# Performance work log

Hardware: AMD Instinct MI355X
Metric: run time of the kernel (lower is better)

Reference implementation:

```python
import jax, jax.numpy as jnp
import numpy as np

B, H, W, C = 32, 32, 32, 256


def setup_inputs() -> dict:
    key = jax.random.key(0)
    k1, k2 = jax.random.split(key)
    feats1 = jax.random.normal(k1, (B, H, W, C), dtype=jnp.float32)
    feats2 = jax.random.normal(k2, (B, H, W, C), dtype=jnp.float32)
    return {"feats1": feats1, "feats2": feats2}


def reference(feats1, feats2):
    # Training path of LocalFeatureLoss (trainflag=True)
    b, h, w, c = feats1.shape
    l = h * w
    q = feats1.reshape(b, l, c)  # queries: (B, l, C)
    p = feats2.reshape(b, l, c)  # preds:   (B, l, C)
    # M[b, a, j] = <p[b,a], q[b,j]>  == fm2 @ fm1.T per batch
    M = jnp.einsum('bac,bjc->baj', p, q)  # (B, l_pred, l_query)
    max1 = jnp.argmax(M, axis=1)  # (B, l_q): best pred index for each query token
    max2 = jnp.argmax(M, axis=2)  # (B, l_p): best query index for each pred token
    # mutual nearest-neighbor check: m[b, j] = max2[b, max1[b, j]]
    m = jnp.take_along_axis(max2, max1, axis=1)  # (B, l_q)
    valid = jnp.arange(l)[None, :] == m          # (B, l_q) bool
    # gather matched pred descriptors and compute per-pair similarity
    matched_p = jnp.take_along_axis(p, max1[..., None], axis=1)  # (B, l_q, C)
    sims = jnp.sum(q * matched_p, axis=-1)                        # (B, l_q)
    cnt = jnp.sum(valid, axis=1).astype(sims.dtype)               # (B,)
    # mean over mutual NN pairs (torch mean over idx1)
    similarity = jnp.sum(jnp.where(valid, sims, 0.0), axis=1) / jnp.maximum(cnt, 1.0)
    return similarity
```

## Files before the change

kernel.cpp:

```cpp
#include <hip/hip_runtime.h>
#include <hip/hip_bf16.h>

#define BATCH 32
#define L 1024
#define CD 256
#define NRT 8
#define NCT 16
#define PAN_A 32768
#define TILE_B 16384

typedef __bf16 bf16x8 __attribute__((ext_vector_type(8)));
typedef float  f32x4  __attribute__((ext_vector_type(4)));
typedef unsigned long long u64;

__device__ __forceinline__ unsigned int enc_f32(float f) {
    unsigned int u = __float_as_uint(f);
    return ((int)u < 0) ? ~u : (u | 0x80000000u);
}
__device__ __forceinline__ float dec_f32(unsigned int u) {
    u = (u & 0x80000000u) ? (u & 0x7FFFFFFFu) : ~u;
    return __uint_as_float(u);
}
__device__ __forceinline__ u64 pmax(u64 a, u64 b) { return a > b ? a : b; }

__device__ __forceinline__ void gl_lds16(const __bf16* g, __bf16* l) {
    __builtin_amdgcn_global_load_lds(
        (const __attribute__((address_space(1))) unsigned int*)g,
        (__attribute__((address_space(3))) unsigned int*)l, 16, 0, 0);
}

__global__ __launch_bounds__(256) void convert_kernel(
    const float* __restrict__ qg,
    const float* __restrict__ pg,
    __bf16* __restrict__ qsw,
    __bf16* __restrict__ psw)
{
    const unsigned int t = blockIdx.x * 256 + threadIdx.x;
    const unsigned int v = t & ((1u << 20) - 1);
    const bool isQ = (t >> 20) != 0;

    const float* src;
    __bf16* dst;
    if (isQ) {
        const int s    = v & 7;
        const int row  = (v >> 3) & 63;
        const int step = (v >> 9) & 3;
        const int ct   = (v >> 11) & 15;
        const int b    = v >> 15;
        src = qg + ((size_t)(b * L + ct * 64 + row)) * CD
                 + step * 64 + ((s ^ (row & 7)) * 8);
        dst = qsw + (size_t)v * 8;
    } else {
        const int s    = v & 7;
        const int row  = (v >> 3) & 127;
        const int step = (v >> 10) & 3;
        const int pan  = (v >> 12) & 7;
        const int b    = v >> 15;
        src = pg + ((size_t)(b * L + pan * 128 + row)) * CD
                 + step * 64 + ((s ^ (row & 7)) * 8);
        dst = psw + (size_t)v * 8;
    }
    const float4 f0 = *(const float4*)src;
    const float4 f1 = *(const float4*)(src + 4);
    bf16x8 o;
    o[0] = (__bf16)f0.x; o[1] = (__bf16)f0.y; o[2] = (__bf16)f0.z; o[3] = (__bf16)f0.w;
    o[4] = (__bf16)f1.x; o[5] = (__bf16)f1.y; o[6] = (__bf16)f1.z; o[7] = (__bf16)f1.w;
    *(bf16x8*)&dst[0] = o;
}

__global__ __launch_bounds__(512, 2) void mm_argmax_kernel(
    const __bf16* __restrict__ qsw,
    const __bf16* __restrict__ psw,
    u64* __restrict__ colpart,
    int* __restrict__ max2)
{
    __shared__ __bf16 sA[4 * 8192];
    __shared__ __bf16 sB[2][4 * 4096];
    __shared__ u64 sRow[2][128];

    const int tid = threadIdx.x;
    const int bid = blockIdx.x;
    const int b  = bid & 31;
    const int rt = bid >> 5;

    const int lane = tid & 63;
    const int w    = tid >> 6;
    const int wm   = w >> 1;
    const int wn   = w & 1;
    const int quad = lane >> 4;
    const int l16  = lane & 15;

    const __bf16* pa  = psw + (size_t)(b * NRT + rt) * PAN_A;
    const __bf16* pbb = qsw + (size_t)b * NCT * TILE_B;

    #pragma unroll
    for (int c = 0; c < 8; ++c)
        gl_lds16(pa + c * 4096 + tid * 8, &sA[c * 4096 + tid * 8]);
    #pragma unroll
    for (int c = 0; c < 4; ++c)
        gl_lds16(pbb + c * 4096 + tid * 8, &sB[0][c * 4096 + tid * 8]);
    #pragma unroll
    for (int c = 0; c < 4; ++c)
        gl_lds16(pbb + TILE_B + c * 4096 + tid * 8, &sB[1][c * 4096 + tid * 8]);

    f32x4 acc[2][2];
    float rowv[2][4];
    int   rowj[2][4];
    #pragma unroll
    for (int tm = 0; tm < 2; ++tm)
        #pragma unroll
        for (int r = 0; r < 4; ++r) { rowv[tm][r] = -1e30f; rowj[tm][r] = 0; }

    asm volatile("s_waitcnt vmcnt(4)" ::: "memory");
    __builtin_amdgcn_s_barrier();
    __builtin_amdgcn_sched_barrier(0);

    const size_t colbase = ((size_t)(b * NRT + rt) * 4 + wm) * L;
    const int a0q = rt * 128 + wm * 32 + quad * 4;

    for (int t = 0; t < NCT; ++t) {
        const __bf16* sBb = sB[t & 1];
        #pragma unroll
        for (int tm = 0; tm < 2; ++tm)
            #pragma unroll
            for (int tn = 0; tn < 2; ++tn) acc[tm][tn] = (f32x4){0.f, 0.f, 0.f, 0.f};

        __builtin_amdgcn_s_setprio(1);
        #pragma unroll
        for (int step = 0; step < 4; ++step) {
            #pragma unroll
            for (int kk = 0; kk < 2; ++kk) {
                const int sw = ((kk * 4 + quad) ^ (l16 & 7)) << 3;
                bf16x8 a0 = *(const bf16x8*)&sA [step * 8192 + (wm * 32      + l16) * 64 + sw];
                bf16x8 a1 = *(const bf16x8*)&sA [step * 8192 + (wm * 32 + 16 + l16) * 64 + sw];
                bf16x8 b0 = *(const bf16x8*)&sBb[step * 4096 + (wn * 32      + l16) * 64 + sw];
                bf16x8 b1 = *(const bf16x8*)&sBb[step * 4096 + (wn * 32 + 16 + l16) * 64 + sw];
                acc[0][0] = __builtin_amdgcn_mfma_f32_16x16x32_bf16(a0, b0, acc[0][0], 0, 0, 0);
                acc[0][1] = __builtin_amdgcn_mfma_f32_16x16x32_bf16(a0, b1, acc[0][1], 0, 0, 0);
                acc[1][0] = __builtin_amdgcn_mfma_f32_16x16x32_bf16(a1, b0, acc[1][0], 0, 0, 0);
                acc[1][1] = __builtin_amdgcn_mfma_f32_16x16x32_bf16(a1, b1, acc[1][1], 0, 0, 0);
            }
        }
        __builtin_amdgcn_s_setprio(0);

        const int jb = t * 64 + wn * 32 + l16;
        #pragma unroll
        for (int tm = 0; tm < 2; ++tm)
            #pragma unroll
            for (int r = 0; r < 4; ++r) {
                const float v0 = acc[tm][0][r], v1 = acc[tm][1][r];
                if (v0 > rowv[tm][r]) { rowv[tm][r] = v0; rowj[tm][r] = jb; }
                if (v1 > rowv[tm][r]) { rowv[tm][r] = v1; rowj[tm][r] = jb + 16; }
            }

        #pragma unroll
        for (int tn = 0; tn < 2; ++tn) {
            float cv = acc[0][tn][0];
            int   ca = a0q;
            #pragma unroll
            for (int r = 1; r < 4; ++r)
                if (acc[0][tn][r] > cv) { cv = acc[0][tn][r]; ca = a0q + r; }
            #pragma unroll
            for (int r = 0; r < 4; ++r)
                if (acc[1][tn][r] > cv) { cv = acc[1][tn][r]; ca = a0q + 16 + r; }
            u64 pk = ((u64)enc_f32(cv) << 32) | (unsigned int)(~(unsigned int)ca);
            pk = pmax(pk, __shfl_xor(pk, 16));
            pk = pmax(pk, __shfl_xor(pk, 32));
            if (quad == 0)
                colpart[colbase + t * 64 + wn * 32 + tn * 16 + l16] = pk;
        }

        __builtin_amdgcn_s_barrier();
        __builtin_amdgcn_sched_barrier(0);
        if (t + 2 < NCT) {
            #pragma unroll
            for (int c = 0; c < 4; ++c)
                gl_lds16(pbb + (size_t)(t + 2) * TILE_B + c * 4096 + tid * 8,
                         &sB[t & 1][c * 4096 + tid * 8]);
        }
        if (t < NCT - 1) {
            if (t + 2 < NCT) { asm volatile("s_waitcnt vmcnt(6)" ::: "memory"); }
            else             { asm volatile("s_waitcnt vmcnt(2)" ::: "memory"); }
            __builtin_amdgcn_s_barrier();
            __builtin_amdgcn_sched_barrier(0);
        }
    }

    #pragma unroll
    for (int tm = 0; tm < 2; ++tm)
        #pragma unroll
        for (int r = 0; r < 4; ++r) {
            u64 pk = ((u64)enc_f32(rowv[tm][r]) << 32)
                   | (unsigned int)(~(unsigned int)rowj[tm][r]);
            pk = pmax(pk, __shfl_xor(pk, 1));
            pk = pmax(pk, __shfl_xor(pk, 2));
            pk = pmax(pk, __shfl_xor(pk, 4));
            pk = pmax(pk, __shfl_xor(pk, 8));
            if (l16 == 0) sRow[wn][wm * 32 + tm * 16 + quad * 4 + r] = pk;
        }
    __syncthreads();
    if (tid < 128) {
        const u64 m = pmax(sRow[0][tid], sRow[1][tid]);
        max2[(size_t)b * L + rt * 128 + tid] = (int)(~(unsigned int)m) & (L - 1);
    }
}

__global__ __launch_bounds__(1024) void finalize_kernel(
    const u64* __restrict__ colpart,
    const int* __restrict__ max2,
    float* __restrict__ out)
{
    __shared__ int sMax2[L];
    __shared__ float sSum[16];
    __shared__ int sCnt[16];
    const int b = blockIdx.x;
    const int j = threadIdx.x;

    sMax2[j] = max2[(size_t)b * L + j];

    u64 cb = 0ull;
    #pragma unroll
    for (int k = 0; k < 32; ++k)
        cb = pmax(cb, colpart[((size_t)b * 32 + k) * L + j]);
    __syncthreads();

    const int a = (int)(~(unsigned int)cb) & (L - 1);
    const float val = dec_f32((unsigned int)(cb >> 32));
    const bool mut = (sMax2[a] == j);
    float sum = mut ? val : 0.f;
    int   cnt = mut ? 1 : 0;

    #pragma unroll
    for (int o = 32; o >= 1; o >>= 1) {
        sum += __shfl_down(sum, o);
        cnt += __shfl_down(cnt, o);
    }
    if ((j & 63) == 0) { sSum[j >> 6] = sum; sCnt[j >> 6] = cnt; }
    __syncthreads();
    if (j == 0) {
        float S = 0.f;
        int   C = 0;
        #pragma unroll
        for (int i = 0; i < 16; ++i) { S += sSum[i]; C += sCnt[i]; }
        out[b] = S / fmaxf((float)C, 1.0f);
    }
}

extern "C" void kernel_launch(void* const* d_in, const int* in_sizes, int n_in,
                              void* d_out, int out_size, void* d_ws, size_t ws_size,
                              hipStream_t stream) {
    const float* q = (const float*)d_in[0];
    const float* p = (const float*)d_in[1];
    float* out = (float*)d_out;

    u64* colpart = (u64*)d_ws;
    int* max2 = (int*)(colpart + (size_t)BATCH * 32 * L);
    __bf16* psw = (__bf16*)((char*)d_ws + 8 * 1024 * 1024 + 512 * 1024);
    __bf16* qsw = psw + (size_t)BATCH * NRT * PAN_A;

    convert_kernel<<<8192, 256, 0, stream>>>(q, p, qsw, psw);
    mm_argmax_kernel<<<BATCH * NRT, 512, 0, stream>>>(qsw, psw, colpart, max2);
    finalize_kernel<<<BATCH, 1024, 0, stream>>>(colpart, max2, out);
}
```

Measured before the change: 141.0 us.

## Hold A fragments in registers, widen B tiles, reduce column partials in LDS

The pred (A) panel is pre-laid out by the convert kernel in MFMA fragment order, so each wave loads its 64x256 slice straight into 32 registers instead of staging it in LDS and re-reading it every tile. Waves are rearranged 2x4 with 64 rows each and B tiles grow to 128 columns, giving 8 fully unrolled double-buffered iterations. Column argmax partials are merged across waves in LDS before one write per block, which cuts colpart traffic and the finalize reduction from 32 to 8 entries per column. The cost is much higher register pressure (afr plus acc) under the 512x2 launch bounds, and LDS use goes to 64KB for sB plus 18KB for the reduction buffers, which may spill or lower occupancy.

Measured after the change: 185.2 us. 1.31x slower.

```diff
diff --git a/kernel.cpp b/kernel.cpp
--- a/kernel.cpp
+++ b/kernel.cpp
@@ -5,9 +5,8 @@
 #define L 1024
 #define CD 256
 #define NRT 8
-#define NCT 16
-#define PAN_A 32768
-#define TILE_B 16384
+#define NBT 8
+#define TILE_B 32768
 
 typedef __bf16 bf16x8 __attribute__((ext_vector_type(8)));
 typedef float  f32x4  __attribute__((ext_vector_type(4)));
@@ -33,50 +32,52 @@
     const float* __restrict__ qg,
     const float* __restrict__ pg,
     __bf16* __restrict__ qsw,
-    __bf16* __restrict__ psw)
+    __bf16* __restrict__ areg)
 {
     const unsigned int t = blockIdx.x * 256 + threadIdx.x;
-    const unsigned int v = t & ((1u << 20) - 1);
-    const bool isQ = (t >> 20) != 0;
-
+    const unsigned int v = t & 0xFFFFFu;
     const float* src;
     __bf16* dst;
-    if (isQ) {
+    if (t >> 20) {
         const int s    = v & 7;
-        const int row  = (v >> 3) & 63;
-        const int step = (v >> 9) & 3;
-        const int ct   = (v >> 11) & 15;
+        const int crow = (v >> 3) & 127;
+        const int step = (v >> 10) & 3;
+        const int ct   = (v >> 12) & 7;
         const int b    = v >> 15;
-        src = qg + ((size_t)(b * L + ct * 64 + row)) * CD
-                 + step * 64 + ((s ^ (row & 7)) * 8);
+        src = qg + ((size_t)(b << 10) + (ct << 7) + crow) * CD
+                 + (step << 6) + ((s ^ (crow & 7)) << 3);
         dst = qsw + (size_t)v * 8;
     } else {
-        const int s    = v & 7;
-        const int row  = (v >> 3) & 127;
-        const int step = (v >> 10) & 3;
-        const int pan  = (v >> 12) & 7;
+        const int ln   = v & 63;
+        const int f    = (v >> 6) & 31;
+        const int wmv  = (v >> 11) & 1;
+        const int rtv  = (v >> 12) & 7;
         const int b    = v >> 15;
-        src = pg + ((size_t)(b * L + pan * 128 + row)) * CD
-                 + step * 64 + ((s ^ (row & 7)) * 8);
-        dst = psw + (size_t)v * 8;
+        const int tm   = f >> 3;
+        const int step = (f >> 1) & 3;
+        const int kk   = f & 1;
+        const int row  = (rtv << 7) + (wmv << 6) + (tm << 4) + (ln & 15);
+        const int k    = (step << 6) + (((kk << 2) + (ln >> 4)) << 3);
+        src = pg + ((size_t)(b << 10) + row) * CD + k;
+        dst = areg + (size_t)v * 8;
     }
     const float4 f0 = *(const float4*)src;
     const float4 f1 = *(const float4*)(src + 4);
     bf16x8 o;
     o[0] = (__bf16)f0.x; o[1] = (__bf16)f0.y; o[2] = (__bf16)f0.z; o[3] = (__bf16)f0.w;
     o[4] = (__bf16)f1.x; o[5] = (__bf16)f1.y; o[6] = (__bf16)f1.z; o[7] = (__bf16)f1.w;
-    *(bf16x8*)&dst[0] = o;
+    *(bf16x8*)dst = o;
 }
 
 __global__ __launch_bounds__(512, 2) void mm_argmax_kernel(
     const __bf16* __restrict__ qsw,
-    const __bf16* __restrict__ psw,
+    const __bf16* __restrict__ areg,
     u64* __restrict__ colpart,
     int* __restrict__ max2)
 {
-    __shared__ __bf16 sA[4 * 8192];
-    __shared__ __bf16 sB[2][4 * 4096];
-    __shared__ u64 sRow[2][128];
+    __shared__ __bf16 sB[2][TILE_B];
+    __shared__ u64 sColW[2][L];
+    __shared__ u64 sRowW[4][128];
 
     const int tid = threadIdx.x;
     const int bid = blockIdx.x;
@@ -85,109 +86,122 @@
 
     const int lane = tid & 63;
     const int w    = tid >> 6;
-    const int wm   = w >> 1;
-    const int wn   = w & 1;
+    const int wm   = w >> 2;
+    const int wn   = w & 3;
     const int quad = lane >> 4;
     const int l16  = lane & 15;
 
-    const __bf16* pa  = psw + (size_t)(b * NRT + rt) * PAN_A;
-    const __bf16* pbb = qsw + (size_t)b * NCT * TILE_B;
+    const __bf16* qb = qsw + (size_t)b * NBT * TILE_B;
+    const __bf16* ab = areg + (size_t)((b * NRT + rt) * 2 + wm) * 32 * 512;
+
+    bf16x8 afr[32];
+    #pragma unroll
+    for (int f = 0; f < 32; ++f)
+        afr[f] = *(const bf16x8*)&ab[f * 512 + lane * 8];
+    __builtin_amdgcn_sched_barrier(0);
 
     #pragma unroll
     for (int c = 0; c < 8; ++c)
-        gl_lds16(pa + c * 4096 + tid * 8, &sA[c * 4096 + tid * 8]);
-    #pragma unroll
-    for (int c = 0; c < 4; ++c)
-        gl_lds16(pbb + c * 4096 + tid * 8, &sB[0][c * 4096 + tid * 8]);
-    #pragma unroll
-    for (int c = 0; c < 4; ++c)
-        gl_lds16(pbb + TILE_B + c * 4096 + tid * 8, &sB[1][c * 4096 + tid * 8]);
-
-    f32x4 acc[2][2];
-    float rowv[2][4];
-    int   rowj[2][4];
-    #pragma unroll
-    for (int tm = 0; tm < 2; ++tm)
+        gl_lds16(qb + c * 4096 + tid * 8, &sB[0][c * 4096 + tid * 8]);
+    __builtin_amdgcn_sched_barrier(0);
+    #pragma unroll
+    for (int c = 0; c < 8; ++c)
+        gl_lds16(qb + TILE_B + c * 4096 + tid * 8, &sB[1][c * 4096 + tid * 8]);
+    __builtin_amdgcn_sched_barrier(0);
+
+    f32x4 acc[4][2];
+    float rowv[4][4];
+    int   rowj[4][4];
+    #pragma unroll
+    for (int tm = 0; tm < 4; ++tm)
         #pragma unroll
         for (int r = 0; r < 4; ++r) { rowv[tm][r] = -1e30f; rowj[tm][r] = 0; }
 
-    asm volatile("s_waitcnt vmcnt(4)" ::: "memory");
-    __builtin_amdgcn_s_barrier();
-    __builtin_amdgcn_sched_barrier(0);
-
-    const size_t colbase = ((size_t)(b * NRT + rt) * 4 + wm) * L;
-    const int a0q = rt * 128 + wm * 32 + quad * 4;
-
-    for (int t = 0; t < NCT; ++t) {
-        const __bf16* sBb = sB[t & 1];
-        #pragma unroll
-        for (int tm = 0; tm < 2; ++tm)
-            #pragma unroll
-            for (int tn = 0; tn < 2; ++tn) acc[tm][tn] = (f32x4){0.f, 0.f, 0.f, 0.f};
-
-        __builtin_amdgcn_s_setprio(1);
-        #pragma unroll
-        for (int step = 0; step < 4; ++step) {
-            #pragma unroll
-            for (int kk = 0; kk < 2; ++kk) {
-                const int sw = ((kk * 4 + quad) ^ (l16 & 7)) << 3;
-                bf16x8 a0 = *(const bf16x8*)&sA [step * 8192 + (wm * 32      + l16) * 64 + sw];
-                bf16x8 a1 = *(const bf16x8*)&sA [step * 8192 + (wm * 32 + 16 + l16) * 64 + sw];
-                bf16x8 b0 = *(const bf16x8*)&sBb[step * 4096 + (wn * 32      + l16) * 64 + sw];
-                bf16x8 b1 = *(const bf16x8*)&sBb[step * 4096 + (wn * 32 + 16 + l16) * 64 + sw];
-                acc[0][0] = __builtin_amdgcn_mfma_f32_16x16x32_bf16(a0, b0, acc[0][0], 0, 0, 0);
-                acc[0][1] = __builtin_amdgcn_mfma_f32_16x16x32_bf16(a0, b1, acc[0][1], 0, 0, 0);
-                acc[1][0] = __builtin_amdgcn_mfma_f32_16x16x32_bf16(a1, b0, acc[1][0], 0, 0, 0);
-                acc[1][1] = __builtin_amdgcn_mfma_f32_16x16x32_bf16(a1, b1, acc[1][1], 0, 0, 0);
-            }
+    const int a0q = rt * 128 + wm * 64 + quad * 4;
+
+    #define COMPUTE(T)                                                         \
+    {                                                                          \
+        const __bf16* sBb = sB[(T) & 1];                                       \
+        _Pragma("unroll")                                                      \
+        for (int tm = 0; tm < 4; ++tm)                                         \
+            _Pragma("unroll")                                                  \
+            for (int tn = 0; tn < 2; ++tn) acc[tm][tn] = (f32x4){0.f,0.f,0.f,0.f}; \
+        __builtin_amdgcn_s_setprio(1);                                         \
+        _Pragma("unroll")                                                      \
+        for (int step = 0; step < 4; ++step) {                                 \
+            _Pragma("unroll")                                                  \
+            for (int kk = 0; kk < 2; ++kk) {                                   \
+                const int sw = ((kk * 4 + quad) ^ (l16 & 7)) << 3;             \
+                bf16x8 b0 = *(const bf16x8*)&sBb[step * 8192 + (wn * 32      + l16) * 64 + sw]; \
+                bf16x8 b1 = *(const bf16x8*)&sBb[step * 8192 + (wn * 32 + 16 + l16) * 64 + sw]; \
+                _Pragma("unroll")                                              \
+                for (int tm = 0; tm < 4; ++tm) {                               \
+                    acc[tm][0] = __builtin_amdgcn_mfma_f32_16x16x32_bf16(      \
+                        afr[tm * 8 + step * 2 + kk], b0, acc[tm][0], 0, 0, 0); \
+                    acc[tm][1] = __builtin_amdgcn_mfma_f32_16x16x32_bf16(      \
+                        afr[tm * 8 + step * 2 + kk], b1, acc[tm][1], 0, 0, 0); \
+                }                                                              \
+            }                                                                  \
+        }                                                                      \
+        __builtin_amdgcn_s_setprio(0);                                         \
+         \
+        const int jb = (T) * 128 + wn * 32 + l16;                              \
+        _Pragma("unroll")                                                      \
+        for (int tm = 0; tm < 4; ++tm)                                         \
+            _Pragma("unroll")                                                  \
+            for (int r = 0; r < 4; ++r) {                                      \
+                const float v0 = acc[tm][0][r], v1 = acc[tm][1][r];            \
+                if (v0 > rowv[tm][r]) { rowv[tm][r] = v0; rowj[tm][r] = jb; }  \
+                if (v1 > rowv[tm][r]) { rowv[tm][r] = v1; rowj[tm][r] = jb + 16; } \
+            }                                                                  \
+          \
+        _Pragma("unroll")                                                      \
+        for (int tn = 0; tn < 2; ++tn) {                                       \
+            float cv = acc[0][tn][0];                                          \
+            int   ca = a0q;                                                    \
+            _Pragma("unroll")                                                  \
+            for (int tm = 0; tm < 4; ++tm)                                     \
+                _Pragma("unroll")                                              \
+                for (int r = 0; r < 4; ++r) {                                  \
+                    if (tm == 0 && r == 0) continue;                           \
+                    if (acc[tm][tn][r] > cv) { cv = acc[tm][tn][r]; ca = a0q + tm * 16 + r; } \
+                }                                                              \
+            u64 pk = ((u64)enc_f32(cv) << 32) | (unsigned int)(~(unsigned int)ca); \
+            pk = pmax(pk, __shfl_xor(pk, 16));                                 \
+            pk = pmax(pk, __shfl_xor(pk, 32));                                 \
+            if (quad == 0) sColW[wm][(T) * 128 + wn * 32 + tn * 16 + l16] = pk; \
+        }                                                                      \
+    }
+
+    #define TILE_ITER(T, VM)                                                   \
+        asm volatile("s_waitcnt vmcnt(" #VM ")" ::: "memory");                 \
+        __builtin_amdgcn_s_barrier();                                          \
+        __builtin_amdgcn_sched_barrier(0);                                     \
+        COMPUTE(T)                                                             \
+        __builtin_amdgcn_s_barrier();                                          \
+        __builtin_amdgcn_sched_barrier(0);                                     \
+        if ((T) + 2 < NBT) {                                                   \
+            _Pragma("unroll")                                                  \
+            for (int c = 0; c < 8; ++c)                                        \
+                gl_lds16(qb + (size_t)((T) + 2) * TILE_B + c * 4096 + tid * 8, \
+                         &sB[(T) & 1][c * 4096 + tid * 8]);                    \
+            __builtin_amdgcn_sched_barrier(0);                                 \
         }
-        __builtin_amdgcn_s_setprio(0);
-
-        const int jb = t * 64 + wn * 32 + l16;
-        #pragma unroll
-        for (int tm = 0; tm < 2; ++tm)
-            #pragma unroll
-            for (int r = 0; r < 4; ++r) {
-                const float v0 = acc[tm][0][r], v1 = acc[tm][1][r];
-                if (v0 > rowv[tm][r]) { rowv[tm][r] = v0; rowj[tm][r] = jb; }
-                if (v1 > rowv[tm][r]) { rowv[tm][r] = v1; rowj[tm][r] = jb + 16; }
-            }
-
-        #pragma unroll
-        for (int tn = 0; tn < 2; ++tn) {
-            float cv = acc[0][tn][0];
-            int   ca = a0q;
-            #pragma unroll
-            for (int r = 1; r < 4; ++r)
-                if (acc[0][tn][r] > cv) { cv = acc[0][tn][r]; ca = a0q + r; }
-            #pragma unroll
-            for (int r = 0; r < 4; ++r)
-                if (acc[1][tn][r] > cv) { cv = acc[1][tn][r]; ca = a0q + 16 + r; }
-            u64 pk = ((u64)enc_f32(cv) << 32) | (unsigned int)(~(unsigned int)ca);
-            pk = pmax(pk, __shfl_xor(pk, 16));
-            pk = pmax(pk, __shfl_xor(pk, 32));
-            if (quad == 0)
-                colpart[colbase + t * 64 + wn * 32 + tn * 16 + l16] = pk;
-        }
-
-        __builtin_amdgcn_s_barrier();
-        __builtin_amdgcn_sched_barrier(0);
-        if (t + 2 < NCT) {
-            #pragma unroll
-            for (int c = 0; c < 4; ++c)
-                gl_lds16(pbb + (size_t)(t + 2) * TILE_B + c * 4096 + tid * 8,
-                         &sB[t & 1][c * 4096 + tid * 8]);
-        }
-        if (t < NCT - 1) {
-            if (t + 2 < NCT) { asm volatile("s_waitcnt vmcnt(6)" ::: "memory"); }
-            else             { asm volatile("s_waitcnt vmcnt(2)" ::: "memory"); }
-            __builtin_amdgcn_s_barrier();
-            __builtin_amdgcn_sched_barrier(0);
-        }
-    }
-
-    #pragma unroll
-    for (int tm = 0; tm < 2; ++tm)
+
+    TILE_ITER(0, 8)
+    TILE_ITER(1, 8)
+    TILE_ITER(2, 8)
+    TILE_ITER(3, 8)
+    TILE_ITER(4, 8)
+    TILE_ITER(5, 8)
+    TILE_ITER(6, 8)
+    TILE_ITER(7, 0)
+
+    #undef TILE_ITER
+    #undef COMPUTE
+
+    #pragma unroll
+    for (int tm = 0; tm < 4; ++tm)
         #pragma unroll
         for (int r = 0; r < 4; ++r) {
             u64 pk = ((u64)enc_f32(rowv[tm][r]) << 32)
@@ -196,12 +210,18 @@
             pk = pmax(pk, __shfl_xor(pk, 2));
             pk = pmax(pk, __shfl_xor(pk, 4));
             pk = pmax(pk, __shfl_xor(pk, 8));
-            if (l16 == 0) sRow[wn][wm * 32 + tm * 16 + quad * 4 + r] = pk;
+            if (l16 == 0) sRowW[wn][wm * 64 + tm * 16 + quad * 4 + r] = pk;
         }
     __syncthreads();
     if (tid < 128) {
-        const u64 m = pmax(sRow[0][tid], sRow[1][tid]);
+        const u64 m = pmax(pmax(sRowW[0][tid], sRowW[1][tid]),
+                           pmax(sRowW[2][tid], sRowW[3][tid]));
         max2[(size_t)b * L + rt * 128 + tid] = (int)(~(unsigned int)m) & (L - 1);
+    }
+    #pragma unroll
+    for (int c0 = 0; c0 < 2; ++c0) {
+        const int c = c0 * 512 + tid;
+        colpart[(size_t)(b * NRT + rt) * L + c] = pmax(sColW[0][c], sColW[1][c]);
     }
 }
 
@@ -220,8 +240,8 @@
 
     u64 cb = 0ull;
     #pragma unroll
-    for (int k = 0; k < 32; ++k)
-        cb = pmax(cb, colpart[((size_t)b * 32 + k) * L + j]);
+    for (int k = 0; k < NRT; ++k)
+        cb = pmax(cb, colpart[(size_t)(b * NRT + k) * L + j]);
     __syncthreads();
 
     const int a = (int)(~(unsigned int)cb) & (L - 1);
@@ -254,11 +274,11 @@
     float* out = (float*)d_out;
 
     u64* colpart = (u64*)d_ws;
-    int* max2 = (int*)(colpart + (size_t)BATCH * 32 * L);
-    __bf16* psw = (__bf16*)((char*)d_ws + 8 * 1024 * 1024 + 512 * 1024);
-    __bf16* qsw = psw + (size_t)BATCH * NRT * PAN_A;
-
-    convert_kernel<<<8192, 256, 0, stream>>>(q, p, qsw, psw);
-    mm_argmax_kernel<<<BATCH * NRT, 512, 0, stream>>>(qsw, psw, colpart, max2);
+    int* max2 = (int*)(colpart + (size_t)BATCH * NRT * L);
+    __bf16* areg = (__bf16*)((char*)d_ws + (2u << 20) + (128u << 10));
+    __bf16* qsw = areg + (size_t)8388608;
+
+    convert_kernel<<<8192, 256, 0, stream>>>(q, p, qsw, areg);
+    mm_argmax_kernel<<<BATCH * NRT, 512, 0, stream>>>(qsw, areg, colpart, max2);
     finalize_kernel<<<BATCH, 1024, 0, stream>>>(colpart, max2, out);
 }
```

## Fuse fp32-to-bf16 conversion into matmul-argmax kernel with register-prefetched Q tiles

Applied to the files above, without the earlier changes.

Removes the separate conversion kernel and its bf16 round trip through global memory. The matmul kernel now loads fp32 feats directly, converts to bf16 in registers, and writes swizzled tiles to LDS. Q tiles are prefetched into registers one K-step ahead. Tiling changes to 64-row pred panels with 256-thread blocks (512 blocks) and 128-column query tiles split over K steps. Each block re-reads and re-converts the Q fp32 data (16x per batch), and the loads go through VGPRs instead of direct-to-LDS, which adds register pressure and barrier stalls.

Result: no change. 142.8 us (+1.3%).

```diff
diff --git a/kernel.cpp b/kernel.cpp
--- a/kernel.cpp
+++ b/kernel.cpp
@@ -4,10 +4,8 @@
 #define BATCH 32
 #define L 1024
 #define CD 256
-#define NRT 8
-#define NCT 16
-#define PAN_A 32768
-#define TILE_B 16384
+#define NRT 16
+#define NQT 32
 
 typedef __bf16 bf16x8 __attribute__((ext_vector_type(8)));
 typedef float  f32x4  __attribute__((ext_vector_type(4)));
@@ -22,61 +20,24 @@
     return __uint_as_float(u);
 }
 __device__ __forceinline__ u64 pmax(u64 a, u64 b) { return a > b ? a : b; }
-
-__device__ __forceinline__ void gl_lds16(const __bf16* g, __bf16* l) {
-    __builtin_amdgcn_global_load_lds(
-        (const __attribute__((address_space(1))) unsigned int*)g,
-        (__attribute__((address_space(3))) unsigned int*)l, 16, 0, 0);
-}
-
-__global__ __launch_bounds__(256) void convert_kernel(
+__device__ __forceinline__ bf16x8 cvt8(float4 a, float4 b) {
+    bf16x8 o;
+    o[0] = (__bf16)a.x; o[1] = (__bf16)a.y; o[2] = (__bf16)a.z; o[3] = (__bf16)a.w;
+    o[4] = (__bf16)b.x; o[5] = (__bf16)b.y; o[6] = (__bf16)b.z; o[7] = (__bf16)b.w;
+    return o;
+}
+
+__global__ void __launch_bounds__(256)
+__attribute__((amdgpu_waves_per_eu(2)))
+mm_argmax_kernel(
     const float* __restrict__ qg,
     const float* __restrict__ pg,
-    __bf16* __restrict__ qsw,
-    __bf16* __restrict__ psw)
-{
-    const unsigned int t = blockIdx.x * 256 + threadIdx.x;
-    const unsigned int v = t & ((1u << 20) - 1);
-    const bool isQ = (t >> 20) != 0;
-
-    const float* src;
-    __bf16* dst;
-    if (isQ) {
-        const int s    = v & 7;
-        const int row  = (v >> 3) & 63;
-        const int step = (v >> 9) & 3;
-        const int ct   = (v >> 11) & 15;
-        const int b    = v >> 15;
-        src = qg + ((size_t)(b * L + ct * 64 + row)) * CD
-                 + step * 64 + ((s ^ (row & 7)) * 8);
-        dst = qsw + (size_t)v * 8;
-    } else {
-        const int s    = v & 7;
-        const int row  = (v >> 3) & 127;
-        const int step = (v >> 10) & 3;
-        const int pan  = (v >> 12) & 7;
-        const int b    = v >> 15;
-        src = pg + ((size_t)(b * L + pan * 128 + row)) * CD
-                 + step * 64 + ((s ^ (row & 7)) * 8);
-        dst = psw + (size_t)v * 8;
-    }
-    const float4 f0 = *(const float4*)src;
-    const float4 f1 = *(const float4*)(src + 4);
-    bf16x8 o;
-    o[0] = (__bf16)f0.x; o[1] = (__bf16)f0.y; o[2] = (__bf16)f0.z; o[3] = (__bf16)f0.w;
-    o[4] = (__bf16)f1.x; o[5] = (__bf16)f1.y; o[6] = (__bf16)f1.z; o[7] = (__bf16)f1.w;
-    *(bf16x8*)&dst[0] = o;
-}
-
-__global__ __launch_bounds__(512, 2) void mm_argmax_kernel(
-    const __bf16* __restrict__ qsw,
-    const __bf16* __restrict__ psw,
     u64* __restrict__ colpart,
     int* __restrict__ max2)
 {
-    __shared__ __bf16 sA[4 * 8192];
-    __shared__ __bf16 sB[2][4 * 4096];
-    __shared__ u64 sRow[2][128];
+    __shared__ __bf16 sA[4 * 4096];
+    __shared__ __bf16 sB[2][8192];
+    __shared__ u64 sRow[2][64];
 
     const int tid = threadIdx.x;
     const int bid = blockIdx.x;
@@ -90,108 +51,163 @@
     const int quad = lane >> 4;
     const int l16  = lane & 15;
 
-    const __bf16* pa  = psw + (size_t)(b * NRT + rt) * PAN_A;
-    const __bf16* pbb = qsw + (size_t)b * NCT * TILE_B;
-
-    #pragma unroll
-    for (int c = 0; c < 8; ++c)
-        gl_lds16(pa + c * 4096 + tid * 8, &sA[c * 4096 + tid * 8]);
-    #pragma unroll
-    for (int c = 0; c < 4; ++c)
-        gl_lds16(pbb + c * 4096 + tid * 8, &sB[0][c * 4096 + tid * 8]);
-    #pragma unroll
-    for (int c = 0; c < 4; ++c)
-        gl_lds16(pbb + TILE_B + c * 4096 + tid * 8, &sB[1][c * 4096 + tid * 8]);
-
-    f32x4 acc[2][2];
-    float rowv[2][4];
-    int   rowj[2][4];
+    const float* pA = pg + ((size_t)b * L + rt * 64) * CD;
+    const float* pQ = qg + (size_t)b * L * CD;
+
+    #pragma unroll
+    for (int pass = 0; pass < 2; ++pass) {
+        float4 t[8];
+        #pragma unroll
+        for (int s = 0; s < 4; ++s) {
+            const int sid = (pass * 4 + s) * 256 + tid;
+            const int row = sid >> 5;
+            const int ks  = (sid >> 3) & 3;
+            const int sl  = sid & 7;
+            const float* src = pA + row * CD + ks * 64 + ((sl ^ (row & 7)) << 3);
+            t[2 * s]     = ((const float4*)src)[0];
+            t[2 * s + 1] = ((const float4*)src)[1];
+        }
+        #pragma unroll
+        for (int s = 0; s < 4; ++s) {
+            const int sid = (pass * 4 + s) * 256 + tid;
+            const int row = sid >> 5;
+            const int ks  = (sid >> 3) & 3;
+            const int sl  = sid & 7;
+            *(bf16x8*)&sA[ks * 4096 + row * 64 + sl * 8] = cvt8(t[2 * s], t[2 * s + 1]);
+        }
+    }
+    {
+        float4 t[8];
+        #pragma unroll
+        for (int s = 0; s < 4; ++s) {
+            const int sid  = s * 256 + tid;
+            const int crow = sid >> 3;
+            const int sl   = sid & 7;
+            const float* src = pQ + (size_t)crow * CD + ((sl ^ (crow & 7)) << 3);
+            t[2 * s]     = ((const float4*)src)[0];
+            t[2 * s + 1] = ((const float4*)src)[1];
+        }
+        #pragma unroll
+        for (int s = 0; s < 4; ++s) {
+            const int sid  = s * 256 + tid;
+            const int crow = sid >> 3;
+            const int sl   = sid & 7;
+            *(bf16x8*)&sB[0][crow * 64 + sl * 8] = cvt8(t[2 * s], t[2 * s + 1]);
+        }
+    }
+
+    f32x4 acc[2][4];
+    u64 rowbest[2][4];
     #pragma unroll
     for (int tm = 0; tm < 2; ++tm)
         #pragma unroll
-        for (int r = 0; r < 4; ++r) { rowv[tm][r] = -1e30f; rowj[tm][r] = 0; }
-
-    asm volatile("s_waitcnt vmcnt(4)" ::: "memory");
-    __builtin_amdgcn_s_barrier();
-    __builtin_amdgcn_sched_barrier(0);
-
-    const size_t colbase = ((size_t)(b * NRT + rt) * 4 + wm) * L;
-    const int a0q = rt * 128 + wm * 32 + quad * 4;
-
-    for (int t = 0; t < NCT; ++t) {
-        const __bf16* sBb = sB[t & 1];
-        #pragma unroll
-        for (int tm = 0; tm < 2; ++tm)
-            #pragma unroll
-            for (int tn = 0; tn < 2; ++tn) acc[tm][tn] = (f32x4){0.f, 0.f, 0.f, 0.f};
-
-        __builtin_amdgcn_s_setprio(1);
-        #pragma unroll
-        for (int step = 0; step < 4; ++step) {
-            #pragma unroll
-            for (int kk = 0; kk < 2; ++kk) {
-                const int sw = ((kk * 4 + quad) ^ (l16 & 7)) << 3;
-                bf16x8 a0 = *(const bf16x8*)&sA [step * 8192 + (wm * 32      + l16) * 64 + sw];
-                bf16x8 a1 = *(const bf16x8*)&sA [step * 8192 + (wm * 32 + 16 + l16) * 64 + sw];
-                bf16x8 b0 = *(const bf16x8*)&sBb[step * 4096 + (wn * 32      + l16) * 64 + sw];
-                bf16x8 b1 = *(const bf16x8*)&sBb[step * 4096 + (wn * 32 + 16 + l16) * 64 + sw];
-                acc[0][0] = __builtin_amdgcn_mfma_f32_16x16x32_bf16(a0, b0, acc[0][0], 0, 0, 0);
-                acc[0][1] = __builtin_amdgcn_mfma_f32_16x16x32_bf16(a0, b1, acc[0][1], 0, 0, 0);
-                acc[1][0] = __builtin_amdgcn_mfma_f32_16x16x32_bf16(a1, b0, acc[1][0], 0, 0, 0);
-                acc[1][1] = __builtin_amdgcn_mfma_f32_16x16x32_bf16(a1, b1, acc[1][1], 0, 0, 0);
-            }
-        }
-        __builtin_amdgcn_s_setprio(0);
-
-        const int jb = t * 64 + wn * 32 + l16;
-        #pragma unroll
-        for (int tm = 0; tm < 2; ++tm)
-            #pragma unroll
-            for (int r = 0; r < 4; ++r) {
-                const float v0 = acc[tm][0][r], v1 = acc[tm][1][r];
-                if (v0 > rowv[tm][r]) { rowv[tm][r] = v0; rowj[tm][r] = jb; }
-                if (v1 > rowv[tm][r]) { rowv[tm][r] = v1; rowj[tm][r] = jb + 16; }
-            }
-
-        #pragma unroll
-        for (int tn = 0; tn < 2; ++tn) {
-            float cv = acc[0][tn][0];
-            int   ca = a0q;
-            #pragma unroll
-            for (int r = 1; r < 4; ++r)
-                if (acc[0][tn][r] > cv) { cv = acc[0][tn][r]; ca = a0q + r; }
-            #pragma unroll
-            for (int r = 0; r < 4; ++r)
-                if (acc[1][tn][r] > cv) { cv = acc[1][tn][r]; ca = a0q + 16 + r; }
-            u64 pk = ((u64)enc_f32(cv) << 32) | (unsigned int)(~(unsigned int)ca);
-            pk = pmax(pk, __shfl_xor(pk, 16));
-            pk = pmax(pk, __shfl_xor(pk, 32));
-            if (quad == 0)
-                colpart[colbase + t * 64 + wn * 32 + tn * 16 + l16] = pk;
-        }
-
+        for (int r = 0; r < 4; ++r) rowbest[tm][r] = 0ull;
+
+    const int a0q = rt * 64 + wm * 32 + quad * 4;
+    const size_t colbase = ((size_t)b * 32 + rt * 2 + wm) * L;
+
+    float4 pf[8];
+
+    #pragma unroll 4
+    for (int t = 0; t < NQT; ++t) {
+        asm volatile("s_waitcnt lgkmcnt(0)" ::: "memory");
         __builtin_amdgcn_s_barrier();
         __builtin_amdgcn_sched_barrier(0);
-        if (t + 2 < NCT) {
-            #pragma unroll
-            for (int c = 0; c < 4; ++c)
-                gl_lds16(pbb + (size_t)(t + 2) * TILE_B + c * 4096 + tid * 8,
-                         &sB[t & 1][c * 4096 + tid * 8]);
-        }
-        if (t < NCT - 1) {
-            if (t + 2 < NCT) { asm volatile("s_waitcnt vmcnt(6)" ::: "memory"); }
-            else             { asm volatile("s_waitcnt vmcnt(2)" ::: "memory"); }
-            __builtin_amdgcn_s_barrier();
+
+        if (t < NQT - 1) {
+            const int pos1 = (t + 1) >> 2, ks1 = (t + 1) & 3;
+            #pragma unroll
+            for (int s = 0; s < 4; ++s) {
+                const int sid  = s * 256 + tid;
+                const int crow = sid >> 3;
+                const int sl   = sid & 7;
+                const float* src = pQ + (size_t)(pos1 * 128 + crow) * CD
+                                 + ks1 * 64 + ((sl ^ (crow & 7)) << 3);
+                pf[2 * s]     = ((const float4*)src)[0];
+                pf[2 * s + 1] = ((const float4*)src)[1];
+            }
             __builtin_amdgcn_sched_barrier(0);
         }
+
+        const int ks = t & 3;
+        const __bf16* sBb = sB[t & 1];
+        if (ks == 0) {
+            #pragma unroll
+            for (int tm = 0; tm < 2; ++tm)
+                #pragma unroll
+                for (int tn = 0; tn < 4; ++tn) acc[tm][tn] = (f32x4){0.f, 0.f, 0.f, 0.f};
+        }
+        __builtin_amdgcn_s_setprio(1);
+        #pragma unroll
+        for (int kk = 0; kk < 2; ++kk) {
+            const int sw = ((kk * 4 + quad) ^ (l16 & 7)) << 3;
+            bf16x8 a0 = *(const bf16x8*)&sA[ks * 4096 + (wm * 32      + l16) * 64 + sw];
+            bf16x8 a1 = *(const bf16x8*)&sA[ks * 4096 + (wm * 32 + 16 + l16) * 64 + sw];
+            bf16x8 b0 = *(const bf16x8*)&sBb[(wn * 64      + l16) * 64 + sw];
+            bf16x8 b1 = *(const bf16x8*)&sBb[(wn * 64 + 16 + l16) * 64 + sw];
+            bf16x8 b2 = *(const bf16x8*)&sBb[(wn * 64 + 32 + l16) * 64 + sw];
+            bf16x8 b3 = *(const bf16x8*)&sBb[(wn * 64 + 48 + l16) * 64 + sw];
+            acc[0][0] = __builtin_amdgcn_mfma_f32_16x16x32_bf16(a0, b0, acc[0][0], 0, 0, 0);
+            acc[0][1] = __builtin_amdgcn_mfma_f32_16x16x32_bf16(a0, b1, acc[0][1], 0, 0, 0);
+            acc[0][2] = __builtin_amdgcn_mfma_f32_16x16x32_bf16(a0, b2, acc[0][2], 0, 0, 0);
+            acc[0][3] = __builtin_amdgcn_mfma_f32_16x16x32_bf16(a0, b3, acc[0][3], 0, 0, 0);
+            acc[1][0] = __builtin_amdgcn_mfma_f32_16x16x32_bf16(a1, b0, acc[1][0], 0, 0, 0);
+            acc[1][1] = __builtin_amdgcn_mfma_f32_16x16x32_bf16(a1, b1, acc[1][1], 0, 0, 0);
+            acc[1][2] = __builtin_amdgcn_mfma_f32_16x16x32_bf16(a1, b2, acc[1][2], 0, 0, 0);
+            acc[1][3] = __builtin_amdgcn_mfma_f32_16x16x32_bf16(a1, b3, acc[1][3], 0, 0, 0);
+        }
+        __builtin_amdgcn_s_setprio(0);
+        __builtin_amdgcn_sched_barrier(0);
+
+        if (t < NQT - 1) {
+            #pragma unroll
+            for (int s = 0; s < 4; ++s) {
+                const int sid  = s * 256 + tid;
+                const int crow = sid >> 3;
+                const int sl   = sid & 7;
+                *(bf16x8*)&sB[(t + 1) & 1][crow * 64 + sl * 8] =
+                    cvt8(pf[2 * s], pf[2 * s + 1]);
+            }
+        }
+
+        if (ks == 3) {
+            const int pos = t >> 2;
+            const int jb = pos * 128 + wn * 64 + l16;
+            #pragma unroll
+            for (int tm = 0; tm < 2; ++tm)
+                #pragma unroll
+                for (int r = 0; r < 4; ++r)
+                    #pragma unroll
+                    for (int tn = 0; tn < 4; ++tn) {
+                        const u64 pk = ((u64)enc_f32(acc[tm][tn][r]) << 32)
+                                     | (unsigned int)(~(unsigned int)(jb + tn * 16));
+                        rowbest[tm][r] = pmax(rowbest[tm][r], pk);
+                    }
+            #pragma unroll
+            for (int tn = 0; tn < 4; ++tn) {
+                float cv = acc[0][tn][0];
+                int   ca = a0q;
+                #pragma unroll
+                for (int tm = 0; tm < 2; ++tm)
+                    #pragma unroll
+                    for (int r = 0; r < 4; ++r) {
+                        if (tm == 0 && r == 0) continue;
+                        if (acc[tm][tn][r] > cv) { cv = acc[tm][tn][r]; ca = a0q + tm * 16 + r; }
+                    }
+                u64 pk = ((u64)enc_f32(cv) << 32) | (unsigned int)(~(unsigned int)ca);
+                pk = pmax(pk, __shfl_xor(pk, 16));
+                pk = pmax(pk, __shfl_xor(pk, 32));
+                if (quad == 0)
+                    colpart[colbase + pos * 128 + wn * 64 + tn * 16 + l16] = pk;
+            }
+        }
     }
 
     #pragma unroll
     for (int tm = 0; tm < 2; ++tm)
         #pragma unroll
         for (int r = 0; r < 4; ++r) {
-            u64 pk = ((u64)enc_f32(rowv[tm][r]) << 32)
-                   | (unsigned int)(~(unsigned int)rowj[tm][r]);
+            u64 pk = rowbest[tm][r];
             pk = pmax(pk, __shfl_xor(pk, 1));
             pk = pmax(pk, __shfl_xor(pk, 2));
             pk = pmax(pk, __shfl_xor(pk, 4));
@@ -199,9 +215,9 @@
             if (l16 == 0) sRow[wn][wm * 32 + tm * 16 + quad * 4 + r] = pk;
         }
     __syncthreads();
-    if (tid < 128) {
+    if (tid < 64) {
         const u64 m = pmax(sRow[0][tid], sRow[1][tid]);
-        max2[(size_t)b * L + rt * 128 + tid] = (int)(~(unsigned int)m) & (L - 1);
+        max2[(size_t)b * L + rt * 64 + tid] = (int)(~(unsigned int)m) & (L - 1);
     }
 }
 
@@ -255,10 +271,7 @@
 
     u64* colpart = (u64*)d_ws;
     int* max2 = (int*)(colpart + (size_t)BATCH * 32 * L);
-    __bf16* psw = (__bf16*)((char*)d_ws + 8 * 1024 * 1024 + 512 * 1024);
-    __bf16* qsw = psw + (size_t)BATCH * NRT * PAN_A;
-
-    convert_kernel<<<8192, 256, 0, stream>>>(q, p, qsw, psw);
-    mm_argmax_kernel<<<BATCH * NRT, 512, 0, stream>>>(qsw, psw, colpart, max2);
+
+    mm_argmax_kernel<<<BATCH * NRT, 256, 0, stream>>>(q, p, colpart, max2);
     finalize_kernel<<<BATCH, 1024, 0, stream>>>(colpart, max2, out);
 }
```
